# Kernel optimization log

Hardware: AMD Instinct MI355X
Metric: run time of the kernel (lower is better)

The kernel has to match this reference:

```python
import jax, jax.numpy as jnp
from jax import lax
import numpy as np

GRIDS = [40, 36, 24, 16, 12]
STRIDES = [4, 8, 16, 32, 64]
SCORE_THR = 0.3
MASK_THR = 0.5
UPDATE_THR = 0.05
SIGMA = 2.0
NMS_PRE = 500
MAX_PER_IMG = 30
E = 128            # ins_out_channels -> kernel_out_channels
HF = WF = 128      # seg feature map; upsampled_size_out = 4*HF = 512
IMG_H = IMG_W = 512
ORI_H = ORI_W = 512

# per-candidate stride, matching the cumsum-based fill in get_seg_single
STRIDE_PER_CELL = np.repeat(np.array(STRIDES, np.float32), [g * g for g in GRIDS])  # [3872]


def setup_inputs() -> dict:
    key = jax.random.key(0)
    ks = jax.random.split(key, 11)
    d = {}
    for i, g in enumerate(GRIDS):
        d[f"cate{i}"] = jax.random.uniform(ks[i], (1, g, g, 1), jnp.float32)
        d[f"kern{i}"] = jax.random.normal(ks[5 + i], (1, E, g, g), jnp.float32)
    d["seg_pred"] = jax.random.normal(ks[10], (1, E, HF, WF), jnp.float32)
    return d


def _forward_scores_and_masks(cates, kerns, seg_pred):
    # flatten all FPN levels, exactly mirroring view(-1,C)/permute(1,2,0).view(-1,E)
    scores = jnp.concatenate([c[0].reshape(-1) for c in cates])                 # [M]
    kernels = jnp.concatenate([k[0].transpose(1, 2, 0).reshape(-1, E) for k in kerns])  # [M,E]
    strides = jnp.asarray(STRIDE_PER_CELL)
    valid = scores > SCORE_THR                                                  # score_thr filter (as mask)

    # dynamic 1x1 conv over mask features == channel contraction
    seg_preds = jax.nn.sigmoid(jnp.einsum('me,ehw->mhw', kernels, seg_pred[0]))  # [M,HF,WF]
    seg_masks = seg_preds > MASK_THR
    sum_masks = seg_masks.sum((1, 2)).astype(jnp.float32)
    keep = valid & (sum_masks > strides)
    seg_scores = (seg_preds * seg_masks).sum((1, 2)) / jnp.maximum(sum_masks, 1.0)
    cscores = jnp.where(keep, scores * seg_scores, 0.0)

    # descending sort + truncate to nms_pre (dropped candidates carry score 0)
    top_scores, top_idx = lax.top_k(cscores, NMS_PRE)
    masks_k = seg_masks[top_idx].reshape(NMS_PRE, -1).astype(jnp.float32)       # [N,HW]
    sm = sum_masks[top_idx]

    # matrix NMS (single foreground class -> label matrix = triu of ones)
    inter = masks_k @ masks_k.T                                                 # [N,N]
    union = sm[None, :] + sm[:, None] - inter
    iou = jnp.triu(inter / jnp.maximum(union, 1.0), k=1)
    comp = iou.max(0)                              # max IoU with any higher-scored mask
    decay = jnp.exp(-SIGMA * (iou ** 2 - comp[:, None] ** 2))
    decay_coeff = decay.min(0)
    nms_scores = top_scores * decay_coeff
    nms_scores = jnp.where(nms_scores >= UPDATE_THR, nms_scores, 0.0)           # update_thr filter

    final_scores, fidx = lax.top_k(nms_scores, MAX_PER_IMG)
    sel = top_idx[fidx]
    sel_preds = seg_preds[sel]                                                  # [K,HF,WF]
    up = jax.image.resize(sel_preds, (MAX_PER_IMG, HF * 4, WF * 4), 'bilinear')  # align_corners=False
    up = up[:, :IMG_H, :IMG_W]
    up = jax.image.resize(up, (MAX_PER_IMG, ORI_H, ORI_W), 'bilinear')
    return final_scores, up


def reference(cate0, cate1, cate2, cate3, cate4,
              kern0, kern1, kern2, kern3, kern4, seg_pred):
    cates = [cate0, cate1, cate2, cate3, cate4]
    kerns = [kern0, kern1, kern2, kern3, kern4]
    final_scores, up = _forward_scores_and_masks(cates, kerns, seg_pred)
    seg_label = up > MASK_THR                                                   # [K,H,W]
    vis = final_scores > SCORE_THR                                              # vis_inds in forward()

    # masks_to_boxes, vectorized; invalid/empty rows zeroed (fixed-size output)
    any_x = seg_label.any(1)                                                    # [K,W]
    any_y = seg_label.any(2)                                                    # [K,H]
    xs = jnp.arange(ORI_W)
    ys = jnp.arange(ORI_H)
    xmin = jnp.min(jnp.where(any_x, xs, ORI_W), axis=1)
    xmax = jnp.max(jnp.where(any_x, xs, -1), axis=1)
    ymin = jnp.min(jnp.where(any_y, ys, ORI_H), axis=1)
    ymax = jnp.max(jnp.where(any_y, ys, -1), axis=1)
    boxes = jnp.stack([xmin, ymin, xmax, ymax], -1).astype(jnp.float32)         # [K,4]
    boxes = jnp.where(vis[:, None], boxes, 0.0)
    return boxes, final_scores, vis.astype(jnp.float32)
```

## Files before the change

### kernel.cpp

```cpp
#include <hip/hip_runtime.h>
#include <math.h>

#define M_CELLS 3872
#define M_PAD   3968
#define NPIX    16384

typedef _Float16 half8 __attribute__((ext_vector_type(8)));
typedef float f32x4 __attribute__((ext_vector_type(4)));

#define GL2LDS(g, l) __builtin_amdgcn_global_load_lds( \
    (const __attribute__((address_space(1))) unsigned int*)(g), \
    (__attribute__((address_space(3))) unsigned int*)(l), 16, 0, 0)


static constexpr size_t ALN(size_t x){ return (x + 255) & ~(size_t)255; }

static constexpr size_t F_KF   = 0;
static constexpr size_t F_SC   = F_KF + (size_t)M_CELLS*128*4;
static constexpr size_t F_SM   = F_SC + (size_t)M_CELLS*4;
static constexpr size_t F_CS   = F_SM + (size_t)M_CELLS*4;
static constexpr size_t F_BIT  = F_CS + (size_t)M_CELLS*4;
static constexpr size_t F_SPP  = F_BIT + (size_t)M_CELLS*256*8;
static constexpr size_t F_TIDX = F_SPP + (size_t)64*M_CELLS*4;
static constexpr size_t F_TSC  = F_TIDX + 512*4;
static constexpr size_t F_SMT  = F_TSC + 512*4;
static constexpr size_t F_IOU  = F_SMT + 512*4;
static constexpr size_t F_COMP = F_IOU + (size_t)500*500*4;
static constexpr size_t F_NMS  = F_COMP + 512*4;
static constexpr size_t F_SEL  = F_NMS + 512*4;
static constexpr size_t F_SELP = F_SEL + 32*4;
static constexpr size_t F_RMN  = ALN(F_SELP + (size_t)30*NPIX*4);
static constexpr size_t F_RMX  = F_RMN + 30*512*4;
static constexpr size_t F_KEYS = ALN(F_RMX + 30*512*4);
static constexpr size_t WS_FB  = F_KEYS + 4096*8;

static constexpr size_t B_KF   = 0;
static constexpr size_t B_AFR  = ALN(B_KF  + (size_t)M_PAD*128*4);
static constexpr size_t B_BFR  = ALN(B_AFR + (size_t)31*4096*16);
static constexpr size_t B_SC   = ALN(B_BFR + (size_t)128*4096*16);
static constexpr size_t B_SM   = ALN(B_SC + (size_t)M_PAD*4);
static constexpr size_t B_CS   = ALN(B_SM + (size_t)M_PAD*4);
static constexpr size_t B_BIT  = ALN(B_CS + (size_t)M_PAD*4);
static constexpr size_t B_SPP  = ALN(B_BIT + (size_t)M_PAD*256*8);
static constexpr size_t B_TIDX = ALN(B_SPP + (size_t)128*M_PAD*4);
static constexpr size_t B_TSC  = ALN(B_TIDX + 512*4);
static constexpr size_t B_SMT  = ALN(B_TSC + 512*4);
static constexpr size_t B_IOU  = ALN(B_SMT + 512*4);
static constexpr size_t B_COMP = ALN(B_IOU + (size_t)500*500*4);
static constexpr size_t B_NMS  = ALN(B_COMP + 512*4);
static constexpr size_t B_SEL  = ALN(B_NMS + 512*4);
static constexpr size_t B_SELP = ALN(B_SEL + 32*4);
static constexpr size_t B_RMN  = ALN(B_SELP + (size_t)30*NPIX*4);
static constexpr size_t B_RMX  = B_RMN + 30*512*4;
static constexpr size_t B_CMAP = ALN(B_RMX + 30*512*4);
static constexpr size_t B_RMAP = B_CMAP + 4096*4;
static constexpr size_t B_VCNT = B_RMAP + 4096*4;
static constexpr size_t B_KEYS = ALN(B_VCNT + 64*4);
static constexpr size_t B_AF30 = ALN(B_KEYS + 4096*8);
static constexpr size_t WS_MFMA = B_AF30 + 8*128*16;

__device__ inline unsigned long long packkey(float v, int i) {
  return ((unsigned long long)__float_as_uint(v) << 32) | (unsigned)(0xFFFFFFFFu - (unsigned)i);
}

__global__ __launch_bounds__(256) void k0aT_gather(
    const float* __restrict__ c0,const float* __restrict__ c1,const float* __restrict__ c2,
    const float* __restrict__ c3,const float* __restrict__ c4,
    const float* __restrict__ w0,const float* __restrict__ w1,const float* __restrict__ w2,
    const float* __restrict__ w3,const float* __restrict__ w4,
    float* __restrict__ kfT, float* __restrict__ scores) {
  const int lvl = blockIdx.y;
  const int Gs[5]   = {1600,1296,576,256,144};
  const int offs[5] = {0,1600,2896,3472,3728};
  const int G = Gs[lvl], off = offs[lvl];
  const float* kl = (lvl==0)?w0:(lvl==1)?w1:(lvl==2)?w2:(lvl==3)?w3:w4;
  const float* cl = (lvl==0)?c0:(lvl==1)?c1:(lvl==2)?c2:(lvl==3)?c3:c4;
  int t = blockIdx.x*256 + threadIdx.x;
  if (t >= G*128) return;
  int e = t / G, c = t - e*G;
  kfT[(size_t)e*M_PAD + off + c] = kl[t];
  if (e == 0) scores[off + c] = cl[c];
}

__global__ __launch_bounds__(1024) void k0s_scan(const float* __restrict__ scores,
                                                 int* __restrict__ cmap, int* __restrict__ rmap,
                                                 int* __restrict__ vcnt) {
  __shared__ int ps[1024];
  int tid = threadIdx.x;
  int base = tid*4;
  bool v[4]; int cnt = 0;
  #pragma unroll
  for (int j=0;j<4;j++) {
    int cell = base+j;
    v[j] = (cell < M_CELLS) && (scores[cell] > 0.3f);
    cnt += v[j] ? 1 : 0;
  }
  ps[tid] = cnt;
  __syncthreads();
  for (int off=1; off<1024; off<<=1) {
    int x = (tid >= off) ? ps[tid-off] : 0;
    __syncthreads();
    ps[tid] += x;
    __syncthreads();
  }
  int run = ps[tid] - cnt;
  #pragma unroll
  for (int j=0;j<4;j++) {
    int cell = base+j;
    if (cell < M_CELLS) {
      if (v[j]) { cmap[run] = cell; rmap[cell] = run; run++; }
      else rmap[cell] = -1;
    }
  }
  if (tid == 1023) vcnt[0] = ps[1023];
}

__global__ __launch_bounds__(256) void k0a_gather(
    const float* __restrict__ c0,const float* __restrict__ c1,const float* __restrict__ c2,
    const float* __restrict__ c3,const float* __restrict__ c4,
    const float* __restrict__ w0,const float* __restrict__ w1,const float* __restrict__ w2,
    const float* __restrict__ w3,const float* __restrict__ w4,
    float* __restrict__ kf, float* __restrict__ scores) {
  const int lvl = blockIdx.y;
  const int Gs[5]   = {1600,1296,576,256,144};
  const int offs[5] = {0,1600,2896,3472,3728};
  const int G = Gs[lvl], off = offs[lvl];
  const float* kl = (lvl==0)?w0:(lvl==1)?w1:(lvl==2)?w2:(lvl==3)?w3:w4;
  const float* cl = (lvl==0)?c0:(lvl==1)?c1:(lvl==2)?c2:(lvl==3)?c3:c4;
  int t = blockIdx.x*256 + threadIdx.x;
  if (t >= G*128) return;
  int e = t / G, c = t - e*G;
  kf[(size_t)(off+c)*128 + e] = kl[t];
  if (e == 0) scores[off+c] = cl[c];
}

__global__ __launch_bounds__(256) void k0b_afrag(const float* __restrict__ kfT,
                                                 const int* __restrict__ cmap,
                                                 const int* __restrict__ vcnt,
                                                 _Float16* __restrict__ Af) {
  int P = blockIdx.x*256 + threadIdx.x;
  int mblock = P >> 12;
  int r  = P & 4095;
  int sub = r >> 9, pc = r & 511;
  int ks = sub >> 1, h = sub & 1;
  int mn = pc >> 6, ln = pc & 63;
  int mcomp = mblock*128 + mn*16 + (ln & 15);
  int kb = ks*32 + (ln >> 4)*8;
  half8 o;
  if (mcomp < vcnt[0]) {
    const float* src = kfT + cmap[mcomp];
    #pragma unroll
    for (int j=0;j<8;j++) {
      float x = src[(size_t)(kb+j)*M_PAD];
      _Float16 hi = (_Float16)x;
      o[j] = h ? (_Float16)(x - (float)hi) : hi;
    }
  } else {
    #pragma unroll
    for (int j=0;j<8;j++) o[j] = (_Float16)0.f;
  }
  *(half8*)&Af[(size_t)P*8] = o;
}

__global__ __launch_bounds__(256) void k0c_bfrag(const float* __restrict__ seg,
                                                 _Float16* __restrict__ Bf) {
  int P = blockIdx.x*256 + threadIdx.x;
  int nb = P >> 12;
  int r  = P & 4095;
  int sub = r >> 9, pc = r & 511;
  int ks = sub >> 1, h = sub & 1;
  int mn = pc >> 6, ln = pc & 63;
  int px = nb*128 + mn*16 + (ln & 15);
  int kb = ks*32 + (ln >> 4)*8;
  half8 o;
  #pragma unroll
  for (int j=0;j<8;j++) {
    float x = seg[(size_t)(kb+j)*NPIX + px];
    _Float16 hi = (_Float16)x;
    o[j] = h ? (_Float16)(x - (float)hi) : hi;
  }
  *(half8*)&Bf[(size_t)P*8] = o;
}

__global__ __launch_bounds__(256, 6) void k1_gemm(
    const float* __restrict__ kf, const float* __restrict__ seg,
    unsigned long long* __restrict__ bits, float* __restrict__ spp) {
  int tid = threadIdx.x;
  int p  = blockIdx.x*256 + tid;
  int c0 = blockIdx.y*32;
  float acc[32];
  #pragma unroll
  for (int c=0;c<32;c++) acc[c]=0.f;
  for (int ch=0; ch<8; ch++) {
    float s[16];
    #pragma unroll
    for (int e=0;e<16;e++) s[e] = seg[(size_t)(ch*16+e)*NPIX + p];
    #pragma unroll
    for (int c=0;c<32;c++) {
      float a=0.f;
      #pragma unroll
      for (int e=0;e<16;e++) a = fmaf(kf[(size_t)(c0+c)*128 + ch*16 + e], s[e], a);
      acc[c] += a;
    }
  }
  int wv = tid>>6, ln = tid&63;
  __shared__ float wsum[32][4];
  #pragma unroll
  for (int c=0;c<32;c++) {
    float logit = acc[c];
    bool msk = logit > 0.f;
    unsigned long long bal = __ballot(msk);
    float pr = msk ? __fdividef(1.f, 1.f + __expf(-logit)) : 0.f;
    #pragma unroll
    for (int o=32;o>0;o>>=1) pr += __shfl_down(pr, o);
    if (ln==0) {
      bits[(size_t)(c0+c)*256 + blockIdx.x*4 + wv] = bal;
      wsum[c][wv] = pr;
    }
  }
  __syncthreads();
  if (tid < 32)
    spp[(size_t)blockIdx.x*M_CELLS + c0 + tid] = wsum[tid][0]+wsum[tid][1]+wsum[tid][2]+wsum[tid][3];
}

__global__ __launch_bounds__(256, 4) void k1_mfma(
    const _Float16* __restrict__ Af, const _Float16* __restrict__ Bf,
    const int* __restrict__ vcnt,
    unsigned long long* __restrict__ bits, float* __restrict__ spp) {
  const int n   = blockIdx.x + 31*blockIdx.y;
  const int xcd = n & 7;
  const int idx = n >> 3;
  const int mb  = idx % 31;
  const int nb  = (xcd << 4) + idx / 31;
  if (mb*128 >= vcnt[0]) return;
  __shared__ char lds[32768];
  const int tid  = threadIdx.x;
  const int lane = tid & 63;
  const int wave = tid >> 6;
  const int wr = wave >> 1, wc = wave & 1;
  const char* gA = (const char*)Af + (size_t)mb*65536;
  const char* gB = (const char*)Bf + (size_t)nb*65536;

  f32x4 acc[4][4];
  #pragma unroll
  for (int a=0;a<4;a++)
    #pragma unroll
    for (int b=0;b<4;b++) acc[a][b] = (f32x4){0.f,0.f,0.f,0.f};

  auto issue = [&](int sub, int buf) {
    const char* ga = gA + sub*8192;
    const char* gb = gB + sub*8192;
    char* la = &lds[buf*16384];
    char* lb = &lds[buf*16384 + 8192];
    GL2LDS(ga +  wave   *1024 + lane*16, la +  wave   *1024);
    GL2LDS(ga + (wave+4)*1024 + lane*16, la + (wave+4)*1024);
    GL2LDS(gb +  wave   *1024 + lane*16, lb +  wave   *1024);
    GL2LDS(gb + (wave+4)*1024 + lane*16, lb + (wave+4)*1024);
  };

  issue(0, 0);
  half8 ah[4], bh[4];
  #pragma unroll
  for (int s=0; s<8; s++) {
    __syncthreads();
    if (s < 7) issue(s+1, (s+1)&1);
    const char* lb_ = &lds[(s&1)*16384];
    if ((s & 1) == 0) {
      #pragma unroll
      for (int mt=0; mt<4; mt++) ah[mt] = *(const half8*)&lb_[(wr*4+mt)*1024 + lane*16];
      #pragma unroll
      for (int nt=0; nt<4; nt++) bh[nt] = *(const half8*)&lb_[8192 + (wc*4+nt)*1024 + lane*16];
      #pragma unroll
      for (int nt=0; nt<4; nt++)
        #pragma unroll
        for (int mt=0; mt<4; mt++)
          acc[mt][nt] = __builtin_amdgcn_mfma_f32_16x16x32_f16(ah[mt], bh[nt], acc[mt][nt], 0, 0, 0);
    } else {
      #pragma unroll
      for (int nt=0; nt<4; nt++) {
        half8 bl = *(const half8*)&lb_[8192 + (wc*4+nt)*1024 + lane*16];
        #pragma unroll
        for (int mt=0; mt<4; mt++)
          acc[mt][nt] = __builtin_amdgcn_mfma_f32_16x16x32_f16(ah[mt], bl, acc[mt][nt], 0, 0, 0);
      }
      #pragma unroll
      for (int mt=0; mt<4; mt++) {
        half8 al = *(const half8*)&lb_[(wr*4+mt)*1024 + lane*16];
        #pragma unroll
        for (int nt=0; nt<4; nt++)
          acc[mt][nt] = __builtin_amdgcn_mfma_f32_16x16x32_f16(al, bh[nt], acc[mt][nt], 0, 0, 0);
      }
    }
  }
  __syncthreads();

  const int q = lane >> 4, mm = lane & 15;
  const int mbase = mb * 128;
  const int wordIdx = nb*2 + wc;
  float* ldsf = (float*)lds;
  #pragma unroll
  for (int mt=0; mt<4; mt++) {
    #pragma unroll
    for (int reg=0; reg<4; reg++) {
      unsigned long long bal[4];
      float ps = 0.f;
      #pragma unroll
      for (int nt=0; nt<4; nt++) {
        float lg = acc[mt][nt][reg];
        bal[nt] = __ballot(lg > 0.f);
        if (lg > 0.f) ps += __fdividef(1.f, 1.f + __expf(-lg));
      }
      ps += __shfl_xor(ps, 1); ps += __shfl_xor(ps, 2);
      ps += __shfl_xor(ps, 4); ps += __shfl_xor(ps, 8);
      if (mm == 0) {
        int cl = wr*64 + mt*16 + q*4 + reg;
        unsigned long long wd = 0;
        #pragma unroll
        for (int nt=0; nt<4; nt++)
          wd |= ((bal[nt] >> (q*16)) & 0xFFFFull) << (nt*16);
        bits[(size_t)(mbase + cl)*256 + wordIdx] = wd;
        ldsf[cl*2 + wc] = ps;
      }
    }
  }
  __syncthreads();
  if (tid < 128)
    spp[(size_t)nb*M_PAD + mbase + tid] = ldsf[tid*2] + ldsf[tid*2+1];
}

__global__ __launch_bounds__(256) void k2c_cscore(
    const unsigned long long* __restrict__ bits, const float* __restrict__ spp,
    const float* __restrict__ scores, const int* __restrict__ rmap,
    float* __restrict__ summ, float* __restrict__ cs) {
  int cell = blockIdx.x*4 + (threadIdx.x>>6);
  int ln = threadIdx.x & 63;
  int ridx = rmap[cell];
  if (ridx < 0) { if (ln==0) { summ[cell]=0.f; cs[cell]=0.f; } return; }
  const unsigned long long* row = bits + (size_t)ridx*256;
  int cnt = 0;
  #pragma unroll
  for (int k=0;k<4;k++) cnt += __popcll(row[ln + 64*k]);
  float sp = 0.f;
  for (int i=ln; i<128; i+=64) sp += spp[(size_t)i*M_PAD + ridx];
  #pragma unroll
  for (int o=32;o>0;o>>=1) { cnt += __shfl_down(cnt,o); sp += __shfl_down(sp,o); }
  if (ln==0) {
    float smf = (float)cnt;
    float sc = scores[cell];
    float strd = (cell<1600)?4.f:(cell<2896)?8.f:(cell<3472)?16.f:(cell<3728)?32.f:64.f;
    bool keep = (smf > strd);
    float ss = sp / fmaxf(smf, 1.f);
    summ[cell] = smf;
    cs[cell] = keep ? sc*ss : 0.f;
  }
}

__global__ __launch_bounds__(256) void k2_cscore(
    const unsigned long long* __restrict__ bits, const float* __restrict__ spp,
    const float* __restrict__ scores, float* __restrict__ summ, float* __restrict__ cs,
    int nparts, int mp) {
  int cell = blockIdx.x*4 + (threadIdx.x>>6);
  int ln = threadIdx.x & 63;
  const unsigned long long* row = bits + (size_t)cell*256;
  int cnt = 0;
  #pragma unroll
  for (int k=0;k<4;k++) cnt += __popcll(row[ln + 64*k]);
  float sp = 0.f;
  for (int i=ln; i<nparts; i+=64) sp += spp[(size_t)i*mp + cell];
  #pragma unroll
  for (int o=32;o>0;o>>=1) { cnt += __shfl_down(cnt,o); sp += __shfl_down(sp,o); }
  if (ln==0) {
    float smf = (float)cnt;
    float sc = scores[cell];
    float strd = (cell<1600)?4.f:(cell<2896)?8.f:(cell<3472)?16.f:(cell<3728)?32.f:64.f;
    bool keep = (sc > 0.3f) && (smf > strd);
    float ss = sp / fmaxf(smf, 1.f);
    summ[cell] = smf;
    cs[cell] = keep ? sc*ss : 0.f;
  }
}

__global__ __launch_bounds__(256) void k3a_sort512(const float* __restrict__ cs,
                                                   unsigned long long* __restrict__ keys) {
  __shared__ unsigned long long key[512];
  int b = blockIdx.x, tid = threadIdx.x;
  for (int i=tid;i<512;i+=256) {
    int gi = b*512 + i;
    key[i] = (gi < M_CELLS) ? packkey(cs[gi], gi) : 0ULL;
  }
  __syncthreads();
  for (int size=2; size<=512; size<<=1) {
    for (int st=size>>1; st>0; st>>=1) {
      for (int i=tid;i<512;i+=256) {
        int pp = i ^ st;
        if (pp > i) {
          unsigned long long a=key[i], bb=key[pp];
          bool desc = (((b*512+i) & size) == 0);
          if (desc ? (a<bb) : (a>bb)) { key[i]=bb; key[pp]=a; }
        }
      }
      __syncthreads();
    }
  }
  for (int i=tid;i<512;i+=256) keys[b*512+i] = key[i];
}

__global__ __launch_bounds__(1024) void k3b_merge(const unsigned long long* __restrict__ keys,
    const float* __restrict__ summ,
    int* __restrict__ tidx, float* __restrict__ tsc, float* __restrict__ smt) {
  __shared__ unsigned long long key[4096];
  int tid = threadIdx.x;
  for (int i=tid;i<4096;i+=1024) key[i] = keys[i];
  __syncthreads();
  for (int size=1024; size<=4096; size<<=1) {
    for (int st=size>>1; st>0; st>>=1) {
      for (int i=tid;i<4096;i+=1024) {
        int pp = i ^ st;
        if (pp > i) {
          unsigned long long a=key[i], b=key[pp];
          bool desc = ((i & size) == 0);
          if (desc ? (a<b) : (a>b)) { key[i]=b; key[pp]=a; }
        }
      }
      __syncthreads();
    }
  }
  if (tid < 512) {
    if (tid < 500) {
      unsigned long long k = key[tid];
      int idx = (int)(0xFFFFFFFFu - (unsigned)(k & 0xFFFFFFFFull));
      tidx[tid] = idx;
      tsc[tid] = __uint_as_float((unsigned)(k>>32));
      smt[tid] = summ[idx];
    } else { tidx[tid]=0; tsc[tid]=0.f; smt[tid]=0.f; }
  }
}

__global__ __launch_bounds__(256) void k4_iou(
    const unsigned long long* __restrict__ bits, const int* __restrict__ tidx,
    const int* __restrict__ rmap, const float* __restrict__ smt, float* __restrict__ iou) {
  int ti = blockIdx.y, tj = blockIdx.x;
  int tid = threadIdx.x;
  int ty = tid>>4, tx = tid&15;
  int i = ti*16+ty, j = tj*16+tx;
  if (ti > tj) { if (i<500 && j<500) iou[i*500+j] = 0.f; return; }
  __shared__ unsigned long long A[16][130];
  __shared__ unsigned long long B[16][130];
  __shared__ float sa[16], sb[16];
  if (tid<16) sa[tid] = (ti*16+tid<500) ? smt[ti*16+tid] : 0.f;
  else if (tid<32) sb[tid-16] = (tj*16+tid-16<500) ? smt[tj*16+tid-16] : 0.f;
  int inter = 0;
  for (int half=0; half<2; half++) {
    __syncthreads();
    for (int t=tid;t<2048;t+=256) {
      int r=t>>7, k=t&127;
      int ii = ti*16+r;
      int jj = tj*16+r;
      int ri = (ii<500) ? (rmap ? max(rmap[tidx[ii]],0) : tidx[ii]) : 0;
      int rj = (jj<500) ? (rmap ? max(rmap[tidx[jj]],0) : tidx[jj]) : 0;
      A[r][k] = (ii<500) ? bits[(size_t)ri*256 + half*128 + k] : 0ULL;
      B[r][k] = (jj<500) ? bits[(size_t)rj*256 + half*128 + k] : 0ULL;
    }
    __syncthreads();
    for (int k=0;k<128;k++) inter += __popcll(A[ty][k] & B[tx][k]);
  }
  if (i<500 && j<500) {
    float fi = (float)inter;
    float un = sa[ty] + sb[tx] - fi;
    iou[i*500+j] = (i<j) ? fi / fmaxf(un, 1.f) : 0.f;
  }
}

__global__ __launch_bounds__(256) void k56_decay(
    const float* __restrict__ iou, const float* __restrict__ tsc, float* __restrict__ nms) {
  __shared__ float csh[512];
  int tid = threadIdx.x;
  for (int c = tid; c < 512; c += 256) {
    float m0=0.f, m1=0.f, m2=0.f, m3=0.f;
    if (c < 500) {
      int r = 0;
      for (; r+3 < 500; r += 4) {
        m0 = fmaxf(m0, iou[(r  )*500 + c]);
        m1 = fmaxf(m1, iou[(r+1)*500 + c]);
        m2 = fmaxf(m2, iou[(r+2)*500 + c]);
        m3 = fmaxf(m3, iou[(r+3)*500 + c]);
      }
      for (; r < 500; r++) m0 = fmaxf(m0, iou[r*500 + c]);
    }
    csh[c] = fmaxf(fmaxf(m0,m1), fmaxf(m2,m3));
  }
  __syncthreads();
  int tx = tid & 63, ty = tid >> 6;
  int j = blockIdx.x*64 + tx;
  float t0=-1e30f, t1=-1e30f, t2=-1e30f, t3=-1e30f;
  if (j < 500) {
    int i = ty;
    for (; i+12 < 500; i += 16) {
      float v0 = iou[(i   )*500 + j], c0 = csh[i];
      float v1 = iou[(i+ 4)*500 + j], c1 = csh[i+4];
      float v2 = iou[(i+ 8)*500 + j], c2 = csh[i+8];
      float v3 = iou[(i+12)*500 + j], c3 = csh[i+12];
      t0 = fmaxf(t0, v0*v0 - c0*c0);
      t1 = fmaxf(t1, v1*v1 - c1*c1);
      t2 = fmaxf(t2, v2*v2 - c2*c2);
      t3 = fmaxf(t3, v3*v3 - c3*c3);
    }
    for (; i < 500; i += 4) { float v = iou[i*500 + j]; float c = csh[i]; t0 = fmaxf(t0, v*v - c*c); }
  }
  float t = fmaxf(fmaxf(t0,t1), fmaxf(t2,t3));
  __shared__ float red[4][64];
  red[ty][tx] = t;
  __syncthreads();
  if (ty == 0 && j < 512) {
    float out = 0.f;
    if (j < 500) {
      float tt = fmaxf(fmaxf(red[0][tx],red[1][tx]), fmaxf(red[2][tx],red[3][tx]));
      float s = tsc[j] * __expf(-2.f*tt);
      out = (s >= 0.05f) ? s : 0.f;
    }
    nms[j] = out;
  }
}

__global__ __launch_bounds__(256) void k7_top30(
    const float* __restrict__ nms, const int* __restrict__ tidx,
    int* __restrict__ sel, float* __restrict__ out,
    const float* __restrict__ kfT, _Float16* __restrict__ Af30) {
  __shared__ unsigned long long key[512];
  __shared__ int selsh[30];
  int tid = threadIdx.x;
  for (int i=tid;i<512;i+=256) key[i] = (i<500) ? packkey(nms[i], i) : 0ULL;
  __syncthreads();
  for (int size=2; size<=512; size<<=1) {
    for (int st=size>>1; st>0; st>>=1) {
      for (int i=tid;i<512;i+=256) {
        int pp = i ^ st;
        if (pp > i) {
          unsigned long long a=key[i], b=key[pp];
          bool desc = ((i & size) == 0);
          if (desc ? (a<b) : (a>b)) { key[i]=b; key[pp]=a; }
        }
      }
      __syncthreads();
    }
  }
  if (tid < 30) {
    unsigned long long k = key[tid];
    int j = (int)(0xFFFFFFFFu - (unsigned)(k & 0xFFFFFFFFull));
    float v = __uint_as_float((unsigned)(k>>32));
    out[120+tid] = v;
    out[150+tid] = (v > 0.3f) ? 1.f : 0.f;
    sel[tid] = tidx[j];
    selsh[tid] = tidx[j];
  }
  __syncthreads();
  if (kfT) {
    for (int P = tid; P < 1024; P += 256) {
      int sub = P >> 7, pc = P & 127;
      int ks = sub >> 1, h = sub & 1;
      int mn = pc >> 6, ln = pc & 63;
      int m  = mn*16 + (ln & 15);
      int kb = ks*32 + (ln >> 4)*8;
      half8 o;
      if (m < 30) {
        const float* src = kfT + selsh[m];
        #pragma unroll
        for (int j=0;j<8;j++) {
          float x = src[(size_t)(kb+j)*M_PAD];
          _Float16 hi = (_Float16)x;
          o[j] = h ? (_Float16)(x - (float)hi) : hi;
        }
      } else {
        #pragma unroll
        for (int j=0;j<8;j++) o[j] = (_Float16)0.f;
      }
      *(half8*)&Af30[(size_t)P*8] = o;
    }
  }
}

__global__ __launch_bounds__(256) void k8_mfma(const _Float16* __restrict__ Af30,
                                               const _Float16* __restrict__ Bf,
                                               float* __restrict__ selp) {
  const int nb = blockIdx.x;
  const int lane = threadIdx.x & 63;
  const int w = threadIdx.x >> 6;
  const half8* A = (const half8*)Af30;
  const half8* B = (const half8*)Bf + (size_t)nb*4096;
  f32x4 acc[2][2];
  #pragma unroll
  for (int a=0;a<2;a++)
    #pragma unroll
    for (int b=0;b<2;b++) acc[a][b] = (f32x4){0.f,0.f,0.f,0.f};
  #pragma unroll
  for (int ks=0; ks<4; ks++) {
    half8 ah[2], bh[2], al[2], bl[2];
    #pragma unroll
    for (int mt=0; mt<2; mt++) ah[mt] = A[(ks*2+0)*128 + mt*64 + lane];
    #pragma unroll
    for (int nt=0; nt<2; nt++) bh[nt] = B[(size_t)(ks*2+0)*512 + (w*2+nt)*64 + lane];
    #pragma unroll
    for (int mt=0; mt<2; mt++) al[mt] = A[(ks*2+1)*128 + mt*64 + lane];
    #pragma unroll
    for (int nt=0; nt<2; nt++) bl[nt] = B[(size_t)(ks*2+1)*512 + (w*2+nt)*64 + lane];
    #pragma unroll
    for (int nt=0; nt<2; nt++)
      #pragma unroll
      for (int mt=0; mt<2; mt++) {
        acc[mt][nt] = __builtin_amdgcn_mfma_f32_16x16x32_f16(ah[mt], bh[nt], acc[mt][nt], 0, 0, 0);
        acc[mt][nt] = __builtin_amdgcn_mfma_f32_16x16x32_f16(ah[mt], bl[nt], acc[mt][nt], 0, 0, 0);
        acc[mt][nt] = __builtin_amdgcn_mfma_f32_16x16x32_f16(al[mt], bh[nt], acc[mt][nt], 0, 0, 0);
      }
  }
  const int q = lane >> 4, col = lane & 15;
  #pragma unroll
  for (int mt=0; mt<2; mt++)
    #pragma unroll
    for (int nt=0; nt<2; nt++)
      #pragma unroll
      for (int reg=0; reg<4; reg++) {
        int m = mt*16 + q*4 + reg;
        if (m < 30) {
          int px = nb*128 + w*32 + nt*16 + col;
          float lg = acc[mt][nt][reg];
          selp[(size_t)m*NPIX + px] = __fdividef(1.f, 1.f + __expf(-lg));
        }
      }
}

__global__ __launch_bounds__(256) void k8_selp(
    const float* __restrict__ kf, const float* __restrict__ seg,
    const int* __restrict__ sel, float* __restrict__ selp) {
  int px = blockIdx.x*256 + threadIdx.x;
  int cells[30];
  #pragma unroll
  for (int m=0;m<30;m++) cells[m] = __builtin_amdgcn_readfirstlane(sel[m]);
  float acc[30];
  #pragma unroll
  for (int m=0;m<30;m++) acc[m] = 0.f;
  for (int e=0; e<128; e+=4) {
    float s0 = seg[(size_t)(e+0)*NPIX + px];
    float s1 = seg[(size_t)(e+1)*NPIX + px];
    float s2 = seg[(size_t)(e+2)*NPIX + px];
    float s3 = seg[(size_t)(e+3)*NPIX + px];
    #pragma unroll
    for (int m=0;m<30;m++) {
      const float* kr = kf + (size_t)cells[m]*128 + e;
      acc[m] = fmaf(kr[0], s0, fmaf(kr[1], s1, fmaf(kr[2], s2, fmaf(kr[3], s3, acc[m]))));
    }
  }
  #pragma unroll
  for (int m=0;m<30;m++)
    selp[(size_t)m*NPIX + px] = __fdividef(1.f, 1.f + __expf(-acc[m]));
}

__global__ __launch_bounds__(256) void k9a_rows(const float* __restrict__ selp,
                                               int* __restrict__ rowmn, int* __restrict__ rowmx) {
  int msk = blockIdx.y, oy = blockIdx.x;
  const float* mp = selp + (size_t)msk*NPIX;
  __shared__ float rows[2][128];
  __shared__ int wmn[4], wmx[4];
  int tid = threadIdx.x;
  float yf = fminf(fmaxf((oy+0.5f)*0.25f - 0.5f, 0.f), 127.f);
  int y0 = (int)yf, y1 = min(y0+1,127);
  float fy = yf-(float)y0;
  if (tid < 128) rows[0][tid] = mp[y0*128 + tid];
  else           rows[1][tid-128] = mp[y1*128 + tid-128];
  __syncthreads();
  int mnx = 512, mxx = -1;
  #pragma unroll
  for (int h=0; h<2; h++) {
    int ox = tid + h*256;
    float xf = fminf(fmaxf((ox+0.5f)*0.25f - 0.5f, 0.f), 127.f);
    int x0 = (int)xf, x1 = min(x0+1,127);
    float fx = xf-(float)x0;
    float v0 = rows[0][x0]*(1.f-fx) + rows[0][x1]*fx;
    float v1 = rows[1][x0]*(1.f-fx) + rows[1][x1]*fx;
    float v  = v0*(1.f-fy) + v1*fy;
    if (v > 0.5f) { mnx = min(mnx, ox); mxx = max(mxx, ox); }
  }
  #pragma unroll
  for (int o=32;o>0;o>>=1) {
    mnx = min(mnx, __shfl_down(mnx, o));
    mxx = max(mxx, __shfl_down(mxx, o));
  }
  if ((tid & 63) == 0) { wmn[tid>>6] = mnx; wmx[tid>>6] = mxx; }
  __syncthreads();
  if (tid == 0) {
    rowmn[msk*512 + oy] = min(min(wmn[0],wmn[1]), min(wmn[2],wmn[3]));
    rowmx[msk*512 + oy] = max(max(wmx[0],wmx[1]), max(wmx[2],wmx[3]));
  }
}

__global__ __launch_bounds__(512) void k9b_box(const int* __restrict__ rowmn,
                                              const int* __restrict__ rowmx, float* out) {
  int msk = blockIdx.x, tid = threadIdx.x;
  __shared__ int r0[512], r1[512], r2[512], r3[512];
  int mn = rowmn[msk*512 + tid];
  int mx = rowmx[msk*512 + tid];
  bool occ = (mx >= 0);
  r0[tid] = mn;
  r1[tid] = mx;
  r2[tid] = occ ? tid : 512;
  r3[tid] = occ ? tid : -1;
  __syncthreads();
  for (int s=256;s>0;s>>=1) {
    if (tid<s) {
      r0[tid]=min(r0[tid],r0[tid+s]); r1[tid]=max(r1[tid],r1[tid+s]);
      r2[tid]=min(r2[tid],r2[tid+s]); r3[tid]=max(r3[tid],r3[tid+s]);
    }
    __syncthreads();
  }
  if (tid==0) {
    bool vis = out[120+msk] > 0.3f;
    out[msk*4+0] = vis ? (float)r0[0] : 0.f;
    out[msk*4+1] = vis ? (float)r2[0] : 0.f;
    out[msk*4+2] = vis ? (float)r1[0] : 0.f;
    out[msk*4+3] = vis ? (float)r3[0] : 0.f;
  }
}

extern "C" void kernel_launch(void* const* d_in, const int* in_sizes, int n_in,
                              void* d_out, int out_size, void* d_ws, size_t ws_size,
                              hipStream_t stream) {
  (void)in_sizes; (void)n_in; (void)out_size;
  if (ws_size < WS_FB) return;
  const float* cate[5]; const float* kern[5];
  for (int i=0;i<5;i++){ cate[i]=(const float*)d_in[2*i]; kern[i]=(const float*)d_in[2*i+1]; }
  const float* seg = (const float*)d_in[10];
  char* ws = (char*)d_ws;
  float* out = (float*)d_out;

  const bool mfma = (ws_size >= WS_MFMA);

  float* kf      = (float*)(ws + (mfma ? B_KF   : F_KF));
  float* scores  = (float*)(ws + (mfma ? B_SC   : F_SC));
  float* summ    = (float*)(ws + (mfma ? B_SM   : F_SM));
  float* cs      = (float*)(ws + (mfma ? B_CS   : F_CS));
  unsigned long long* bits = (unsigned long long*)(ws + (mfma ? B_BIT : F_BIT));
  float* spp     = (float*)(ws + (mfma ? B_SPP  : F_SPP));
  int*   tidx    = (int*)(ws + (mfma ? B_TIDX : F_TIDX));
  float* tsc     = (float*)(ws + (mfma ? B_TSC  : F_TSC));
  float* smt     = (float*)(ws + (mfma ? B_SMT  : F_SMT));
  float* iou     = (float*)(ws + (mfma ? B_IOU  : F_IOU));
  float* nms     = (float*)(ws + (mfma ? B_NMS  : F_NMS));
  int*   sel     = (int*)(ws + (mfma ? B_SEL  : F_SEL));
  float* selp    = (float*)(ws + (mfma ? B_SELP : F_SELP));
  int*   rowmn   = (int*)(ws + (mfma ? B_RMN  : F_RMN));
  int*   rowmx   = (int*)(ws + (mfma ? B_RMX  : F_RMX));
  unsigned long long* keys = (unsigned long long*)(ws + (mfma ? B_KEYS : F_KEYS));

  if (mfma) {
    _Float16* Af = (_Float16*)(ws + B_AFR);
    _Float16* Bf = (_Float16*)(ws + B_BFR);
    _Float16* Af30 = (_Float16*)(ws + B_AF30);
    int* cmap = (int*)(ws + B_CMAP);
    int* rmap = (int*)(ws + B_RMAP);
    int* vcnt = (int*)(ws + B_VCNT);
    k0aT_gather<<<dim3(800,5), 256, 0, stream>>>(cate[0],cate[1],cate[2],cate[3],cate[4],
                                      kern[0],kern[1],kern[2],kern[3],kern[4],
                                      kf, scores);
    k0s_scan <<<1, 1024, 0, stream>>>(scores, cmap, rmap, vcnt);
    k0c_bfrag<<<128*4096/256, 256, 0, stream>>>(seg, Bf);
    k0b_afrag<<<31*4096/256, 256, 0, stream>>>(kf, cmap, vcnt, Af);
    k1_mfma  <<<dim3(31, 128), 256, 0, stream>>>(Af, Bf, vcnt, bits, spp);
    k2c_cscore<<<M_CELLS/4, 256, 0, stream>>>(bits, spp, scores, rmap, summ, cs);
    k3a_sort512<<<8, 256, 0, stream>>>(cs, keys);
    k3b_merge  <<<1, 1024, 0, stream>>>(keys, summ, tidx, tsc, smt);
    k4_iou   <<<dim3(32,32), 256, 0, stream>>>(bits, tidx, rmap, smt, iou);
    k56_decay<<<8, 256, 0, stream>>>(iou, tsc, nms);
    k7_top30 <<<1, 256, 0, stream>>>(nms, tidx, sel, out, kf, Af30);
    k8_mfma  <<<128, 256, 0, stream>>>(Af30, Bf, selp);
  } else {
    k0a_gather<<<dim3(800,5), 256, 0, stream>>>(cate[0],cate[1],cate[2],cate[3],cate[4],
                                      kern[0],kern[1],kern[2],kern[3],kern[4], kf, scores);
    k1_gemm  <<<dim3(64,121), 256, 0, stream>>>(kf, seg, bits, spp);
    k2_cscore<<<M_CELLS/4, 256, 0, stream>>>(bits, spp, scores, summ, cs, 64, M_CELLS);
    k3a_sort512<<<8, 256, 0, stream>>>(cs, keys);
    k3b_merge  <<<1, 1024, 0, stream>>>(keys, summ, tidx, tsc, smt);
    k4_iou   <<<dim3(32,32), 256, 0, stream>>>(bits, tidx, nullptr, smt, iou);
    k56_decay<<<8, 256, 0, stream>>>(iou, tsc, nms);
    k7_top30 <<<1, 256, 0, stream>>>(nms, tidx, sel, out, nullptr, nullptr);
    k8_selp  <<<NPIX/256, 256, 0, stream>>>(kf, seg, sel, selp);
  }
  k9a_rows <<<dim3(512,30), 256, 0, stream>>>(selp, rowmn, rowmx);
  k9b_box  <<<30, 512, 0, stream>>>(rowmn, rowmx, out);
}
```

Measured before the change: 289.2 us.

## Fuse IoU column max and box reduction into producers via atomics

The IoU kernel now takes a per-column max of the upper-triangular IoU with wave shuffles and writes it to a compensation buffer using atomicMax on the float bit patterns, which are non-negative. The decay kernel therefore no longer scans the 500x500 matrix column by column. The row-extent kernel now folds per-mask min and max extents directly into small aggregate buffers with atomics, so a tiny final kernel replaces the 512-thread reduction kernel. The partial sigmoid sums buffer is transposed so the cscore kernel reads each candidate's values contiguously. In exchange the change adds atomic contention and a buffer initialisation step, which is done in the scan kernel or in a new init kernel on the fallback path.

```diff
diff --git a/kernel.cpp b/kernel.cpp
--- a/kernel.cpp
+++ b/kernel.cpp
@@ -84,9 +84,13 @@
 
 __global__ __launch_bounds__(1024) void k0s_scan(const float* __restrict__ scores,
                                                  int* __restrict__ cmap, int* __restrict__ rmap,
-                                                 int* __restrict__ vcnt) {
+                                                 int* __restrict__ vcnt,
+                                                 unsigned* __restrict__ compU,
+                                                 int* __restrict__ mnAgg, int* __restrict__ mxAgg) {
   __shared__ int ps[1024];
   int tid = threadIdx.x;
+  if (tid < 512) compU[tid] = 0u;
+  if (tid < 60) { mnAgg[tid] = 0x7FFFFFFF; mxAgg[tid] = -1; }
   int base = tid*4;
   bool v[4]; int cnt = 0;
   #pragma unroll
@@ -113,6 +117,13 @@
     }
   }
   if (tid == 1023) vcnt[0] = ps[1023];
+}
+
+__global__ __launch_bounds__(512) void kinit(unsigned* __restrict__ compU,
+                                             int* __restrict__ mnAgg, int* __restrict__ mxAgg) {
+  int tid = threadIdx.x;
+  if (tid < 512) compU[tid] = 0u;
+  if (tid < 60) { mnAgg[tid] = 0x7FFFFFFF; mxAgg[tid] = -1; }
 }
 
 __global__ __launch_bounds__(256) void k0a_gather(
@@ -325,7 +336,7 @@
   }
   __syncthreads();
   if (tid < 128)
-    spp[(size_t)nb*M_PAD + mbase + tid] = ldsf[tid*2] + ldsf[tid*2+1];
+    spp[(size_t)(mbase + tid)*128 + nb] = ldsf[tid*2] + ldsf[tid*2+1];
 }
 
 __global__ __launch_bounds__(256) void k2c_cscore(
@@ -340,8 +351,7 @@
   int cnt = 0;
   #pragma unroll
   for (int k=0;k<4;k++) cnt += __popcll(row[ln + 64*k]);
-  float sp = 0.f;
-  for (int i=ln; i<128; i+=64) sp += spp[(size_t)i*M_PAD + ridx];
+  float sp = spp[(size_t)ridx*128 + ln] + spp[(size_t)ridx*128 + 64 + ln];
   #pragma unroll
   for (int o=32;o>0;o>>=1) { cnt += __shfl_down(cnt,o); sp += __shfl_down(sp,o); }
   if (ln==0) {
@@ -438,7 +448,8 @@
 
 __global__ __launch_bounds__(256) void k4_iou(
     const unsigned long long* __restrict__ bits, const int* __restrict__ tidx,
-    const int* __restrict__ rmap, const float* __restrict__ smt, float* __restrict__ iou) {
+    const int* __restrict__ rmap, const float* __restrict__ smt, float* __restrict__ iou,
+    unsigned* __restrict__ compU) {
   int ti = blockIdx.y, tj = blockIdx.x;
   int tid = threadIdx.x;
   int ty = tid>>4, tx = tid&15;
@@ -464,31 +475,26 @@
     __syncthreads();
     for (int k=0;k<128;k++) inter += __popcll(A[ty][k] & B[tx][k]);
   }
+  float v = 0.f;
   if (i<500 && j<500) {
     float fi = (float)inter;
     float un = sa[ty] + sb[tx] - fi;
-    iou[i*500+j] = (i<j) ? fi / fmaxf(un, 1.f) : 0.f;
-  }
-}
-
-__global__ __launch_bounds__(256) void k56_decay(
-    const float* __restrict__ iou, const float* __restrict__ tsc, float* __restrict__ nms) {
+    v = (i<j) ? fi / fmaxf(un, 1.f) : 0.f;
+    iou[i*500+j] = v;
+  }
+  float cm = v;
+  cm = fmaxf(cm, __shfl_xor(cm, 16));
+  cm = fmaxf(cm, __shfl_xor(cm, 32));
+  if (((tid & 63) < 16) && j < 500 && cm > 0.f)
+    atomicMax(&compU[j], __float_as_uint(cm));
+}
+
+__global__ __launch_bounds__(256) void k6_decay(
+    const float* __restrict__ iou, const float* __restrict__ comp,
+    const float* __restrict__ tsc, float* __restrict__ nms) {
   __shared__ float csh[512];
   int tid = threadIdx.x;
-  for (int c = tid; c < 512; c += 256) {
-    float m0=0.f, m1=0.f, m2=0.f, m3=0.f;
-    if (c < 500) {
-      int r = 0;
-      for (; r+3 < 500; r += 4) {
-        m0 = fmaxf(m0, iou[(r  )*500 + c]);
-        m1 = fmaxf(m1, iou[(r+1)*500 + c]);
-        m2 = fmaxf(m2, iou[(r+2)*500 + c]);
-        m3 = fmaxf(m3, iou[(r+3)*500 + c]);
-      }
-      for (; r < 500; r++) m0 = fmaxf(m0, iou[r*500 + c]);
-    }
-    csh[c] = fmaxf(fmaxf(m0,m1), fmaxf(m2,m3));
-  }
+  for (int i=tid; i<512; i+=256) csh[i] = (i<500) ? comp[i] : 0.f;
   __syncthreads();
   int tx = tid & 63, ty = tid >> 6;
   int j = blockIdx.x*64 + tx;
@@ -655,7 +661,7 @@
 }
 
 __global__ __launch_bounds__(256) void k9a_rows(const float* __restrict__ selp,
-                                               int* __restrict__ rowmn, int* __restrict__ rowmx) {
+                                               int* __restrict__ mnAgg, int* __restrict__ mxAgg) {
   int msk = blockIdx.y, oy = blockIdx.x;
   const float* mp = selp + (size_t)msk*NPIX;
   __shared__ float rows[2][128];
@@ -687,37 +693,30 @@
   if ((tid & 63) == 0) { wmn[tid>>6] = mnx; wmx[tid>>6] = mxx; }
   __syncthreads();
   if (tid == 0) {
-    rowmn[msk*512 + oy] = min(min(wmn[0],wmn[1]), min(wmn[2],wmn[3]));
-    rowmx[msk*512 + oy] = max(max(wmx[0],wmx[1]), max(wmx[2],wmx[3]));
-  }
-}
-
-__global__ __launch_bounds__(512) void k9b_box(const int* __restrict__ rowmn,
-                                              const int* __restrict__ rowmx, float* out) {
-  int msk = blockIdx.x, tid = threadIdx.x;
-  __shared__ int r0[512], r1[512], r2[512], r3[512];
-  int mn = rowmn[msk*512 + tid];
-  int mx = rowmx[msk*512 + tid];
-  bool occ = (mx >= 0);
-  r0[tid] = mn;
-  r1[tid] = mx;
-  r2[tid] = occ ? tid : 512;
-  r3[tid] = occ ? tid : -1;
-  __syncthreads();
-  for (int s=256;s>0;s>>=1) {
-    if (tid<s) {
-      r0[tid]=min(r0[tid],r0[tid+s]); r1[tid]=max(r1[tid],r1[tid+s]);
-      r2[tid]=min(r2[tid],r2[tid+s]); r3[tid]=max(r3[tid],r3[tid+s]);
-    }
-    __syncthreads();
-  }
-  if (tid==0) {
-    bool vis = out[120+msk] > 0.3f;
-    out[msk*4+0] = vis ? (float)r0[0] : 0.f;
-    out[msk*4+1] = vis ? (float)r2[0] : 0.f;
-    out[msk*4+2] = vis ? (float)r1[0] : 0.f;
-    out[msk*4+3] = vis ? (float)r3[0] : 0.f;
-  }
+    int bmn = min(min(wmn[0],wmn[1]), min(wmn[2],wmn[3]));
+    int bmx = max(max(wmx[0],wmx[1]), max(wmx[2],wmx[3]));
+    if (bmx >= 0) {
+      atomicMin(&mnAgg[msk*2+0], bmn);
+      atomicMax(&mxAgg[msk*2+0], bmx);
+      atomicMin(&mnAgg[msk*2+1], oy);
+      atomicMax(&mxAgg[msk*2+1], oy);
+    }
+  }
+}
+
+__global__ __launch_bounds__(64) void k9f_box(const int* __restrict__ mnAgg,
+                                              const int* __restrict__ mxAgg, float* out) {
+  int m = threadIdx.x;
+  if (m >= 30) return;
+  bool vis = out[120+m] > 0.3f;
+  int xmn = min(mnAgg[m*2+0], 512);
+  int ymn = min(mnAgg[m*2+1], 512);
+  int xmx = mxAgg[m*2+0];
+  int ymx = mxAgg[m*2+1];
+  out[m*4+0] = vis ? (float)xmn : 0.f;
+  out[m*4+1] = vis ? (float)ymn : 0.f;
+  out[m*4+2] = vis ? (float)xmx : 0.f;
+  out[m*4+3] = vis ? (float)ymx : 0.f;
 }
 
 extern "C" void kernel_launch(void* const* d_in, const int* in_sizes, int n_in,
@@ -743,11 +742,12 @@
   float* tsc     = (float*)(ws + (mfma ? B_TSC  : F_TSC));
   float* smt     = (float*)(ws + (mfma ? B_SMT  : F_SMT));
   float* iou     = (float*)(ws + (mfma ? B_IOU  : F_IOU));
+  unsigned* compU= (unsigned*)(ws + (mfma ? B_COMP : F_COMP));
   float* nms     = (float*)(ws + (mfma ? B_NMS  : F_NMS));
   int*   sel     = (int*)(ws + (mfma ? B_SEL  : F_SEL));
   float* selp    = (float*)(ws + (mfma ? B_SELP : F_SELP));
-  int*   rowmn   = (int*)(ws + (mfma ? B_RMN  : F_RMN));
-  int*   rowmx   = (int*)(ws + (mfma ? B_RMX  : F_RMX));
+  int*   mnAgg   = (int*)(ws + (mfma ? B_RMN  : F_RMN));
+  int*   mxAgg   = (int*)(ws + (mfma ? B_RMX  : F_RMX));
   unsigned long long* keys = (unsigned long long*)(ws + (mfma ? B_KEYS : F_KEYS));
 
   if (mfma) {
@@ -760,29 +760,30 @@
     k0aT_gather<<<dim3(800,5), 256, 0, stream>>>(cate[0],cate[1],cate[2],cate[3],cate[4],
                                       kern[0],kern[1],kern[2],kern[3],kern[4],
                                       kf, scores);
-    k0s_scan <<<1, 1024, 0, stream>>>(scores, cmap, rmap, vcnt);
+    k0s_scan <<<1, 1024, 0, stream>>>(scores, cmap, rmap, vcnt, compU, mnAgg, mxAgg);
     k0c_bfrag<<<128*4096/256, 256, 0, stream>>>(seg, Bf);
     k0b_afrag<<<31*4096/256, 256, 0, stream>>>(kf, cmap, vcnt, Af);
     k1_mfma  <<<dim3(31, 128), 256, 0, stream>>>(Af, Bf, vcnt, bits, spp);
     k2c_cscore<<<M_CELLS/4, 256, 0, stream>>>(bits, spp, scores, rmap, summ, cs);
     k3a_sort512<<<8, 256, 0, stream>>>(cs, keys);
     k3b_merge  <<<1, 1024, 0, stream>>>(keys, summ, tidx, tsc, smt);
-    k4_iou   <<<dim3(32,32), 256, 0, stream>>>(bits, tidx, rmap, smt, iou);
-    k56_decay<<<8, 256, 0, stream>>>(iou, tsc, nms);
+    k4_iou   <<<dim3(32,32), 256, 0, stream>>>(bits, tidx, rmap, smt, iou, compU);
+    k6_decay <<<8, 256, 0, stream>>>(iou, (const float*)compU, tsc, nms);
     k7_top30 <<<1, 256, 0, stream>>>(nms, tidx, sel, out, kf, Af30);
     k8_mfma  <<<128, 256, 0, stream>>>(Af30, Bf, selp);
   } else {
     k0a_gather<<<dim3(800,5), 256, 0, stream>>>(cate[0],cate[1],cate[2],cate[3],cate[4],
                                       kern[0],kern[1],kern[2],kern[3],kern[4], kf, scores);
+    kinit    <<<1, 512, 0, stream>>>(compU, mnAgg, mxAgg);
     k1_gemm  <<<dim3(64,121), 256, 0, stream>>>(kf, seg, bits, spp);
     k2_cscore<<<M_CELLS/4, 256, 0, stream>>>(bits, spp, scores, summ, cs, 64, M_CELLS);
     k3a_sort512<<<8, 256, 0, stream>>>(cs, keys);
     k3b_merge  <<<1, 1024, 0, stream>>>(keys, summ, tidx, tsc, smt);
-    k4_iou   <<<dim3(32,32), 256, 0, stream>>>(bits, tidx, nullptr, smt, iou);
-    k56_decay<<<8, 256, 0, stream>>>(iou, tsc, nms);
+    k4_iou   <<<dim3(32,32), 256, 0, stream>>>(bits, tidx, nullptr, smt, iou, compU);
+    k6_decay <<<8, 256, 0, stream>>>(iou, (const float*)compU, tsc, nms);
     k7_top30 <<<1, 256, 0, stream>>>(nms, tidx, sel, out, nullptr, nullptr);
     k8_selp  <<<NPIX/256, 256, 0, stream>>>(kf, seg, sel, selp);
   }
-  k9a_rows <<<dim3(512,30), 256, 0, stream>>>(selp, rowmn, rowmx);
-  k9b_box  <<<30, 512, 0, stream>>>(rowmn, rowmx, out);
-}
+  k9a_rows <<<dim3(512,30), 256, 0, stream>>>(selp, mnAgg, mxAgg);
+  k9f_box  <<<1, 64, 0, stream>>>(mnAgg, mxAgg, out);
+}
```

After: 483.5 us. 67.2% more time.
